# Kernel tuning notes

Hardware: AMD Instinct MI355X
Metric: run time of the kernel (lower is better)

## Reference

```python
import jax, jax.numpy as jnp
import numpy as np

N = 50000
E = 800000
IN, HID, OUT, HEADS = 128, 64, 64, 3
NEG_SLOPE = 0.2
BN_EPS = 1e-5


def setup_inputs() -> dict:
    key = jax.random.key(0)
    ks = jax.random.split(key, 20)
    s = 0.05
    inp = {
        "x": jax.random.normal(ks[0], (N, IN), jnp.float32),
        "edge_index": jax.random.randint(ks[1], (2, E), 0, N, jnp.int32),
        # layer 0: in=128 -> heads=3, C=64 (concat -> 192)
        "Wl0": jax.random.normal(ks[2], (IN, HEADS * HID), jnp.float32) * s,
        "bl0": jnp.zeros((HEADS * HID,), jnp.float32),
        "Wr0": jax.random.normal(ks[3], (IN, HEADS * HID), jnp.float32) * s,
        "br0": jnp.zeros((HEADS * HID,), jnp.float32),
        "att0": jax.random.normal(ks[4], (HEADS, HID), jnp.float32) * s,
        "bias0": jnp.zeros((HEADS * HID,), jnp.float32),
        "gamma0": jnp.ones((HEADS * HID,), jnp.float32),
        "beta0": jnp.zeros((HEADS * HID,), jnp.float32),
        # layer 1: in=192 -> heads=1, C=64
        "Wl1": jax.random.normal(ks[5], (HEADS * HID, OUT), jnp.float32) * s,
        "bl1": jnp.zeros((OUT,), jnp.float32),
        "Wr1": jax.random.normal(ks[6], (HEADS * HID, OUT), jnp.float32) * s,
        "br1": jnp.zeros((OUT,), jnp.float32),
        "att1": jax.random.normal(ks[7], (1, OUT), jnp.float32) * s,
        "bias1": jnp.zeros((OUT,), jnp.float32),
        "gamma1": jnp.ones((OUT,), jnp.float32),
        "beta1": jnp.zeros((OUT,), jnp.float32),
    }
    return inp


def _gatv2_layer(x, Wl, bl, Wr, br, att, bias, src, dst, n):
    H, C = att.shape
    xl = (x @ Wl + bl).reshape(n, H, C)
    xr = (x @ Wr + br).reshape(n, H, C)
    e = jax.nn.leaky_relu(xl[src] + xr[dst], NEG_SLOPE)      # [E,H,C]
    logit = jnp.einsum("ehc,hc->eh", e, att)                 # [E,H]
    m = jax.lax.stop_gradient(jax.ops.segment_max(logit, dst, num_segments=n))
    p = jnp.exp(logit - m[dst])
    denom = jax.ops.segment_sum(p, dst, num_segments=n)
    alpha = p / denom[dst]                                   # per-dst softmax
    out = jax.ops.segment_sum(alpha[:, :, None] * xl[src], dst, num_segments=n)
    return out.reshape(n, H * C) + bias


def _bn(x, gamma, beta):
    mu = x.mean(0)
    var = x.var(0)
    return (x - mu) * jax.lax.rsqrt(var + BN_EPS) * gamma + beta


def reference(x, edge_index, Wl0, bl0, Wr0, br0, att0, bias0, gamma0, beta0,
              Wl1, bl1, Wr1, br1, att1, bias1, gamma1, beta1):
    n = x.shape[0]
    loops = jnp.arange(n, dtype=edge_index.dtype)
    src = jnp.concatenate([edge_index[0], loops])  # PyG add_self_loops=True
    dst = jnp.concatenate([edge_index[1], loops])
    h = _gatv2_layer(x, Wl0, bl0, Wr0, br0, att0, bias0, src, dst, n)
    h = _bn(jax.nn.relu(h), gamma0, beta0)
    h = _gatv2_layer(h, Wl1, bl1, Wr1, br1, att1, bias1, src, dst, n)
    h = _bn(jax.nn.relu(h), gamma1, beta1)
    return h
```

## Files before the change

kernel.cpp:

```cpp
#include <hip/hip_runtime.h>
#include <hip/hip_bf16.h>

#define LRELU_SLOPE 0.2f
#define BN_EPS 1e-5f

typedef __attribute__((ext_vector_type(8))) short short8v;
typedef __attribute__((ext_vector_type(4))) float float4v;

static __device__ __forceinline__ unsigned short f2bf(float f) {
    __hip_bfloat16 b = __float2bfloat16(f);
    return *reinterpret_cast<unsigned short*>(&b);
}
static __device__ __forceinline__ void unpack2(unsigned int u, float& f0, float& f1) {
    f0 = __uint_as_float(u << 16);
    f1 = __uint_as_float(u & 0xffff0000u);
}
static __device__ __forceinline__ float lrelu(float x) {
    return fmaxf(x, LRELU_SLOPE * x);
}

__global__ void convert_w2_kernel(const float* __restrict__ Wl0, const float* __restrict__ Wr0,
                                  const float* __restrict__ Wl1, const float* __restrict__ Wr1,
                                  unsigned short* __restrict__ Wt0, unsigned short* __restrict__ Wt1) {
    int idx = blockIdx.x * blockDim.x + threadIdx.x;
    if (idx < 384 * 128) {
        int c = idx >> 7, k = idx & 127;
        float v = (c < 192) ? Wl0[(size_t)k * 192 + c] : Wr0[(size_t)k * 192 + (c - 192)];
        Wt0[idx] = f2bf(v);
    } else if (idx < 384 * 128 + 128 * 192) {
        int i2 = idx - 384 * 128;
        int c = i2 / 192, k = i2 % 192;
        float v = (c < 64) ? Wl1[(size_t)k * 64 + c] : Wr1[(size_t)k * 64 + (c - 64)];
        Wt1[i2] = f2bf(v);
    }
}

__global__ void count_dst_kernel(const int* __restrict__ dst, int* __restrict__ counts, int E) {
    int e = blockIdx.x * blockDim.x + threadIdx.x;
    if (e < E) atomicAdd(&counts[dst[e]], 1);
}

__global__ void scanA_kernel(const int* __restrict__ counts, int* __restrict__ offs,
                             int* __restrict__ blkSum, int n) {
    __shared__ int wsum[4];
    const int lane = threadIdx.x & 63;
    const int wv = threadIdx.x >> 6;
    int i0 = blockIdx.x * 1024 + (int)threadIdx.x * 4;
    int v0 = (i0 + 0 < n) ? counts[i0 + 0] : 0;
    int v1 = (i0 + 1 < n) ? counts[i0 + 1] : 0;
    int v2 = (i0 + 2 < n) ? counts[i0 + 2] : 0;
    int v3 = (i0 + 3 < n) ? counts[i0 + 3] : 0;
    int s4 = v0 + v1 + v2 + v3;
    int s = s4;
    #pragma unroll
    for (int off = 1; off < 64; off <<= 1) {
        int t = __shfl_up(s, off, 64);
        if (lane >= off) s += t;
    }
    if (lane == 63) wsum[wv] = s;
    __syncthreads();
    int wpre = 0;
    for (int w = 0; w < wv; ++w) wpre += wsum[w];
    int excl = wpre + s - s4;
    if (i0 + 0 < n) offs[i0 + 0] = excl;
    excl += v0;
    if (i0 + 1 < n) offs[i0 + 1] = excl;
    excl += v1;
    if (i0 + 2 < n) offs[i0 + 2] = excl;
    excl += v2;
    if (i0 + 3 < n) offs[i0 + 3] = excl;
    if (threadIdx.x == 255) blkSum[blockIdx.x] = wpre + s;
}

__global__ void scanC_kernel(int* __restrict__ offs, const int* __restrict__ blkSum, int n, int E) {
    __shared__ int baseSh;
    const int b = blockIdx.x;
    if (threadIdx.x < 64) {
        int acc = 0;
        for (int i = threadIdx.x; i < b; i += 64) acc += blkSum[i];
        #pragma unroll
        for (int off = 1; off < 64; off <<= 1) acc += __shfl_xor(acc, off, 64);
        if (threadIdx.x == 0) baseSh = acc;
    }
    __syncthreads();
    const int base = baseSh;
    int i = b * 1024 + (int)threadIdx.x * 4;
    if (i + 3 < n) {
        int4 v = *reinterpret_cast<int4*>(&offs[i]);
        v.x += base; v.y += base; v.z += base; v.w += base;
        *reinterpret_cast<int4*>(&offs[i]) = v;
    } else {
        #pragma unroll
        for (int k = 0; k < 4; ++k)
            if (i + k < n) offs[i + k] += base;
    }
    if (b == 0 && threadIdx.x == 0) offs[n] = E;
}

__global__ void scatter_kernel(const int* __restrict__ src, const int* __restrict__ dst,
                               const int* __restrict__ offs, int* __restrict__ cursor,
                               int* __restrict__ esrc, int E) {
    int e = blockIdx.x * blockDim.x + threadIdx.x;
    if (e < E) {
        int d = dst[e];
        int pos = offs[d] + atomicAdd(&cursor[d], 1);
        esrc[pos] = src[e];
    }
}

template <int K, int NCH, bool BN>
__global__ __launch_bounds__(256) void mfma_dual_gemm(
    const float* __restrict__ X,
    const unsigned short* __restrict__ Wt,
    const float* __restrict__ bl, const float* __restrict__ br,
    const float* __restrict__ stats, const float* __restrict__ gamma,
    const float* __restrict__ beta, float invN,
    unsigned short* __restrict__ xlB, unsigned short* __restrict__ xrB, int N) {
    constexpr int LDA = 40;
    const int rowBase = blockIdx.x * 128;
    const int colBase = blockIdx.y * 128;

    __shared__ unsigned short XS[128 * LDA];
    __shared__ unsigned short WS[128 * LDA];
    __shared__ float ssA[K], ssB[K];

    const int tid = threadIdx.x;
    const int lane = tid & 63;
    const int wv = tid >> 6;
    const int lrow = lane & 15;
    const int lk = lane >> 4;

    if (BN) {
        for (int c = tid; c < K; c += 256) {
            float mu = stats[c] * invN;
            float var = stats[K + c] * invN - mu * mu;
            float sc = gamma[c] * rsqrtf(var + BN_EPS);
            ssA[c] = sc;
            ssB[c] = beta[c] - mu * sc;
        }
        __syncthreads();
    }

    float4v acc[2][8];
    #pragma unroll
    for (int i = 0; i < 2; ++i)
        #pragma unroll
        for (int j = 0; j < 8; ++j) acc[i][j] = (float4v){0.f, 0.f, 0.f, 0.f};

    for (int k0 = 0; k0 < K; k0 += 32) {
        {
            int r = tid >> 3;
            int kq = (tid & 7) * 4;
            float4 sc0, sc1;
            if (BN) {
                sc0 = *reinterpret_cast<const float4*>(&ssA[k0 + kq]);
                sc1 = *reinterpret_cast<const float4*>(&ssB[k0 + kq]);
            }
            #pragma unroll
            for (int i = 0; i < 4; ++i) {
                int row = r + 32 * i;
                int gr = rowBase + row;
                float4 v = make_float4(0.f, 0.f, 0.f, 0.f);
                if (gr < N) v = *reinterpret_cast<const float4*>(&X[(size_t)gr * K + k0 + kq]);
                if (BN) {
                    v.x = v.x * sc0.x + sc1.x;
                    v.y = v.y * sc0.y + sc1.y;
                    v.z = v.z * sc0.z + sc1.z;
                    v.w = v.w * sc0.w + sc1.w;
                }
                ushort4 u;
                u.x = f2bf(v.x); u.y = f2bf(v.y); u.z = f2bf(v.z); u.w = f2bf(v.w);
                *reinterpret_cast<ushort4*>(&XS[row * LDA + kq]) = u;
            }
        }
        {
            int c = tid >> 2;
            int kq8 = (tid & 3) * 8;
            #pragma unroll
            for (int i = 0; i < 2; ++i) {
                int col = c + 64 * i;
                uint4 w = *reinterpret_cast<const uint4*>(&Wt[(size_t)(colBase + col) * K + k0 + kq8]);
                *reinterpret_cast<uint4*>(&WS[col * LDA + kq8]) = w;
            }
        }
        __syncthreads();
        short8v aF[2], bF[8];
        #pragma unroll
        for (int rb = 0; rb < 2; ++rb)
            aF[rb] = *reinterpret_cast<const short8v*>(&XS[(wv * 32 + rb * 16 + lrow) * LDA + lk * 8]);
        #pragma unroll
        for (int cb = 0; cb < 8; ++cb)
            bF[cb] = *reinterpret_cast<const short8v*>(&WS[(cb * 16 + lrow) * LDA + lk * 8]);
        #pragma unroll
        for (int rb = 0; rb < 2; ++rb)
            #pragma unroll
            for (int cb = 0; cb < 8; ++cb)
                acc[rb][cb] = __builtin_amdgcn_mfma_f32_16x16x32_bf16(aF[rb], bF[cb], acc[rb][cb], 0, 0, 0);
        __syncthreads();
    }
    #pragma unroll
    for (int cb = 0; cb < 8; ++cb) {
        int cgG = colBase + cb * 16 + lrow;
        bool isR = cgG >= NCH;
        int cc = isR ? cgG - NCH : cgG;
        int hh = cc >> 6;
        int ch = cc & 63;
        float bv = isR ? br[cc] : bl[cc];
        unsigned short* dstB = (isR ? xrB : xlB) + (size_t)hh * N * 64 + ch;
        #pragma unroll
        for (int rb = 0; rb < 2; ++rb) {
            #pragma unroll
            for (int r = 0; r < 4; ++r) {
                int row = rowBase + wv * 32 + rb * 16 + lk * 4 + r;
                if (row < N) dstB[(size_t)row * 64] = f2bf(acc[rb][cb][r] + bv);
            }
        }
    }
}

template <int H>
__global__ __launch_bounds__(256) void gat_agg_head_kernel(
    const unsigned short* __restrict__ xlB,
    const unsigned short* __restrict__ xrB,
    const int* __restrict__ offs, const int* __restrict__ esrc,
    const float* __restrict__ att,
    const float* __restrict__ bias,
    float* __restrict__ outh,
    int N) {
    const int h = blockIdx.y;
    const unsigned short* xl_ = xlB + (size_t)h * N * 64;
    const unsigned short* xr_ = xrB + (size_t)h * N * 64;
    const int lane = threadIdx.x & 63;
    const int node = blockIdx.x * 4 + (threadIdx.x >> 6);
    if (node >= N) return;
    const int j = lane >> 3;
    const int cg = (lane & 7) * 8;

    float xr[8], at[8], acc[8];
    float den = 0.f;
    {
        uint4 u = *reinterpret_cast<const uint4*>(&xr_[(size_t)node * 64 + cg]);
        unpack2(u.x, xr[0], xr[1]); unpack2(u.y, xr[2], xr[3]);
        unpack2(u.z, xr[4], xr[5]); unpack2(u.w, xr[6], xr[7]);
        float4 a0 = *reinterpret_cast<const float4*>(&att[h * 64 + cg]);
        float4 a1 = *reinterpret_cast<const float4*>(&att[h * 64 + cg + 4]);
        at[0] = a0.x; at[1] = a0.y; at[2] = a0.z; at[3] = a0.w;
        at[4] = a1.x; at[5] = a1.y; at[6] = a1.z; at[7] = a1.w;
        #pragma unroll
        for (int c = 0; c < 8; ++c) acc[c] = 0.f;
    }

    const int beg = offs[node];
    const int total = offs[node + 1] - beg + 1;
    uint4 u0, u1;
    {
        int vc = (j < total) ? j : (total - 1);
        int s0 = (vc == 0) ? node : esrc[beg + vc - 1];
        u0 = *reinterpret_cast<const uint4*>(&xl_[(size_t)s0 * 64 + cg]);
        int v1i = j + 8;
        int vc1 = (v1i < total) ? v1i : (total - 1);
        int s1 = (vc1 == 0) ? node : esrc[beg + vc1 - 1];
        u1 = *reinterpret_cast<const uint4*>(&xl_[(size_t)s1 * 64 + cg]);
    }
    for (int t = 0; t < total; t += 8) {
        float xlv[8];
        unpack2(u0.x, xlv[0], xlv[1]); unpack2(u0.y, xlv[2], xlv[3]);
        unpack2(u0.z, xlv[4], xlv[5]); unpack2(u0.w, xlv[6], xlv[7]);
        u0 = u1;
        const int v2 = t + 16 + j;
        if (v2 < total) {
            int s2 = esrc[beg + v2 - 1];
            u1 = *reinterpret_cast<const uint4*>(&xl_[(size_t)s2 * 64 + cg]);
        }
        float s = 0.f;
        #pragma unroll
        for (int c = 0; c < 8; ++c) s += lrelu(xlv[c] + xr[c]) * at[c];
        #pragma unroll
        for (int off = 1; off <= 4; off <<= 1) s += __shfl_xor(s, off, 64);
        const float w = (t + j < total) ? 1.f : 0.f;
        float p = w * __expf(s);
        den += p;
        #pragma unroll
        for (int c = 0; c < 8; ++c) acc[c] += p * xlv[c];
    }

    #pragma unroll
    for (int off = 8; off <= 32; off <<= 1) {
        den += __shfl_xor(den, off, 64);
        #pragma unroll
        for (int c = 0; c < 8; ++c) acc[c] += __shfl_xor(acc[c], off, 64);
    }

    if (j == 0) {
        float inv = 1.f / den;
        float4 b0 = *reinterpret_cast<const float4*>(&bias[h * 64 + cg]);
        float4 b1 = *reinterpret_cast<const float4*>(&bias[h * 64 + cg + 4]);
        float4 o0, o1;
        o0.x = fmaxf(acc[0] * inv + b0.x, 0.f); o0.y = fmaxf(acc[1] * inv + b0.y, 0.f);
        o0.z = fmaxf(acc[2] * inv + b0.z, 0.f); o0.w = fmaxf(acc[3] * inv + b0.w, 0.f);
        o1.x = fmaxf(acc[4] * inv + b1.x, 0.f); o1.y = fmaxf(acc[5] * inv + b1.y, 0.f);
        o1.z = fmaxf(acc[6] * inv + b1.z, 0.f); o1.w = fmaxf(acc[7] * inv + b1.w, 0.f);
        float* orow = &outh[(size_t)node * (H * 64) + h * 64 + cg];
        *reinterpret_cast<float4*>(orow) = o0;
        *reinterpret_cast<float4*>(orow + 4) = o1;
    }
}

template <int CH>
__global__ void bn_stats_kernel(const float* __restrict__ h, float* __restrict__ stats, int N) {
    const int c = threadIdx.x;
    float s = 0.f, q = 0.f;
    for (int r = blockIdx.x; r < N; r += gridDim.x) {
        float v = h[(size_t)r * CH + c];
        s += v;
        q += v * v;
    }
    atomicAdd(&stats[c], s);
    atomicAdd(&stats[CH + c], q);
}

__global__ void bn_finapply64_kernel(float* __restrict__ h, const float* __restrict__ stats,
                                     const float* __restrict__ gamma, const float* __restrict__ beta,
                                     float invN, size_t total4) {
    size_t i = (size_t)blockIdx.x * blockDim.x + threadIdx.x;
    if (i >= total4) return;
    size_t e = i * 4;
    int c = (int)(e & 63);
    float4 v = *reinterpret_cast<float4*>(&h[e]);
    #pragma unroll
    for (int k = 0; k < 4; ++k) {
        float mu = stats[c + k] * invN;
        float var = stats[64 + c + k] * invN - mu * mu;
        float sc = gamma[c + k] * rsqrtf(var + BN_EPS);
        (&v.x)[k] = ((&v.x)[k] - mu) * sc + beta[c + k];
    }
    *reinterpret_cast<float4*>(&h[e]) = v;
}

extern "C" void kernel_launch(void* const* d_in, const int* in_sizes, int n_in,
                              void* d_out, int out_size, void* d_ws, size_t ws_size,
                              hipStream_t stream) {
    const float* x     = (const float*)d_in[0];
    const int*   eidx  = (const int*)d_in[1];
    const float* Wl0   = (const float*)d_in[2];
    const float* bl0   = (const float*)d_in[3];
    const float* Wr0   = (const float*)d_in[4];
    const float* br0   = (const float*)d_in[5];
    const float* att0  = (const float*)d_in[6];
    const float* bias0 = (const float*)d_in[7];
    const float* g0    = (const float*)d_in[8];
    const float* be0   = (const float*)d_in[9];
    const float* Wl1   = (const float*)d_in[10];
    const float* bl1   = (const float*)d_in[11];
    const float* Wr1   = (const float*)d_in[12];
    const float* br1   = (const float*)d_in[13];
    const float* att1  = (const float*)d_in[14];
    const float* bias1 = (const float*)d_in[15];
    const float* g1    = (const float*)d_in[16];
    const float* be1   = (const float*)d_in[17];

    const int N = in_sizes[0] / 128;
    const int E = in_sizes[1] / 2;
    const int* srcIdx = eidx;
    const int* dstIdx = eidx + E;
    const int nChunks = (N + 1023) >> 10;
    const int nGroups = (N + 3) / 4;
    const float invN = 1.f / (float)N;

    char* base = (char*)d_ws;
    auto alloc = [&](size_t bytes) {
        char* p = base;
        base += (bytes + 255) & ~(size_t)255;
        return p;
    };
    unsigned short* projL = (unsigned short*)alloc((size_t)3 * N * 64 * 2);
    unsigned short* projR = (unsigned short*)alloc((size_t)3 * N * 64 * 2);
    float* h0    = (float*)alloc((size_t)N * 192 * 4);
    int*   offs  = (int*)alloc((size_t)(N + 1) * 4);
    int*   esrc  = (int*)alloc((size_t)E * 4);
    int*   blkSum= (int*)alloc((size_t)nChunks * 4);
    unsigned short* Wt0 = (unsigned short*)alloc((size_t)384 * 128 * 2);
    unsigned short* Wt1 = (unsigned short*)alloc((size_t)128 * 192 * 2);
    char* zeroBeg = base;
    int*   counts = (int*)alloc((size_t)N * 4);
    int*   cursor = (int*)alloc((size_t)N * 4);
    float* stats0 = (float*)alloc(384 * 4);
    float* stats1 = (float*)alloc(128 * 4);
    size_t zeroBytes = (size_t)(base - zeroBeg);

    hipMemsetAsync(zeroBeg, 0, zeroBytes, stream);
    convert_w2_kernel<<<(384 * 128 + 128 * 192 + 255) / 256, 256, 0, stream>>>(Wl0, Wr0, Wl1, Wr1, Wt0, Wt1);

    count_dst_kernel<<<(E + 255) / 256, 256, 0, stream>>>(dstIdx, counts, E);
    scanA_kernel<<<nChunks, 256, 0, stream>>>(counts, offs, blkSum, N);
    scanC_kernel<<<nChunks, 256, 0, stream>>>(offs, blkSum, N, E);
    scatter_kernel<<<(E + 255) / 256, 256, 0, stream>>>(srcIdx, dstIdx, offs, cursor, esrc, E);

    {
        dim3 grid((N + 127) / 128, 3);
        mfma_dual_gemm<128, 192, false><<<grid, 256, 0, stream>>>(
            x, Wt0, bl0, br0, nullptr, nullptr, nullptr, 0.f, projL, projR, N);
    }
    {
        dim3 grid(nGroups, 3);
        gat_agg_head_kernel<3><<<grid, 256, 0, stream>>>(projL, projR, offs, esrc, att0, bias0, h0, N);
    }
    bn_stats_kernel<192><<<256, 192, 0, stream>>>(h0, stats0, N);

    {
        dim3 grid((N + 127) / 128, 1);
        mfma_dual_gemm<192, 64, true><<<grid, 256, 0, stream>>>(
            h0, Wt1, bl1, br1, stats0, g0, be0, invN, projL, projR, N);
    }
    float* out = (float*)d_out;
    {
        dim3 grid(nGroups, 1);
        gat_agg_head_kernel<1><<<grid, 256, 0, stream>>>(projL, projR, offs, esrc, att1, bias1, out, N);
    }
    bn_stats_kernel<64><<<256, 64, 0, stream>>>(out, stats1, N);
    {
        size_t tot4 = (size_t)N * 16;
        bn_finapply64_kernel<<<(unsigned)((tot4 + 255) / 256), 256, 0, stream>>>(out, stats1, g1, be1, invN, tot4);
    }
}
```

Baseline: 382.1 us.

## Stage GEMM epilogue through LDS for vectorized stores; fuse weight conversion with degree count

The GEMM epilogue now writes bf16 results into a per-wave LDS tile that reuses the XS/WS shared buffer, then reads 16-byte chunks and stores them to global memory as coalesced uint4 writes instead of scattered 2-byte stores. Separately, the weight-conversion kernel and the destination-count kernel are merged into one launch to save a kernel launch. This costs extra LDS traffic and a reuse of the staging buffer, which relies on the final __syncthreads of the main loop.

```diff
diff --git a/kernel.cpp b/kernel.cpp
--- a/kernel.cpp
+++ b/kernel.cpp
@@ -19,9 +19,10 @@
     return fmaxf(x, LRELU_SLOPE * x);
 }
 
-__global__ void convert_w2_kernel(const float* __restrict__ Wl0, const float* __restrict__ Wr0,
-                                  const float* __restrict__ Wl1, const float* __restrict__ Wr1,
-                                  unsigned short* __restrict__ Wt0, unsigned short* __restrict__ Wt1) {
+__global__ void convcount_kernel(const float* __restrict__ Wl0, const float* __restrict__ Wr0,
+                                 const float* __restrict__ Wl1, const float* __restrict__ Wr1,
+                                 unsigned short* __restrict__ Wt0, unsigned short* __restrict__ Wt1,
+                                 const int* __restrict__ dst, int* __restrict__ counts, int E) {
     int idx = blockIdx.x * blockDim.x + threadIdx.x;
     if (idx < 384 * 128) {
         int c = idx >> 7, k = idx & 127;
@@ -33,11 +34,7 @@
         float v = (c < 64) ? Wl1[(size_t)k * 64 + c] : Wr1[(size_t)k * 64 + (c - 64)];
         Wt1[i2] = f2bf(v);
     }
-}
-
-__global__ void count_dst_kernel(const int* __restrict__ dst, int* __restrict__ counts, int E) {
-    int e = blockIdx.x * blockDim.x + threadIdx.x;
-    if (e < E) atomicAdd(&counts[dst[e]], 1);
+    if (idx < E) atomicAdd(&counts[dst[idx]], 1);
 }
 
 __global__ void scanA_kernel(const int* __restrict__ counts, int* __restrict__ offs,
@@ -120,8 +117,9 @@
     const int rowBase = blockIdx.x * 128;
     const int colBase = blockIdx.y * 128;
 
-    __shared__ unsigned short XS[128 * LDA];
-    __shared__ unsigned short WS[128 * LDA];
+    __shared__ unsigned short SH[16896];
+    unsigned short* XS = SH;
+    unsigned short* WS = SH + 128 * LDA;
     __shared__ float ssA[K], ssB[K];
 
     const int tid = threadIdx.x;
@@ -198,22 +196,38 @@
                 acc[rb][cb] = __builtin_amdgcn_mfma_f32_16x16x32_bf16(aF[rb], bF[cb], acc[rb][cb], 0, 0, 0);
         __syncthreads();
     }
+
+    unsigned short* TR = SH + wv * (32 * 132);
     #pragma unroll
     for (int cb = 0; cb < 8; ++cb) {
         int cgG = colBase + cb * 16 + lrow;
         bool isR = cgG >= NCH;
         int cc = isR ? cgG - NCH : cgG;
-        int hh = cc >> 6;
-        int ch = cc & 63;
         float bv = isR ? br[cc] : bl[cc];
-        unsigned short* dstB = (isR ? xrB : xlB) + (size_t)hh * N * 64 + ch;
         #pragma unroll
         for (int rb = 0; rb < 2; ++rb) {
             #pragma unroll
             for (int r = 0; r < 4; ++r) {
-                int row = rowBase + wv * 32 + rb * 16 + lk * 4 + r;
-                if (row < N) dstB[(size_t)row * 64] = f2bf(acc[rb][cb][r] + bv);
+                int lr = rb * 16 + lk * 4 + r;
+                TR[lr * 132 + cb * 16 + lrow] = f2bf(acc[rb][cb][r] + bv);
             }
+        }
+    }
+    #pragma unroll
+    for (int it = 0; it < 8; ++it) {
+        int idx = it * 64 + lane;
+        int lr = idx >> 4;
+        int ck = (idx & 15) * 8;
+        int grow = rowBase + wv * 32 + lr;
+        if (grow < N) {
+            uint4 v = *reinterpret_cast<const uint4*>(&TR[lr * 132 + ck]);
+            int cgG = colBase + ck;
+            bool isR = cgG >= NCH;
+            int cc = isR ? cgG - NCH : cgG;
+            int hh = cc >> 6;
+            int ch = cc & 63;
+            unsigned short* dstB = (isR ? xrB : xlB) + (size_t)hh * N * 64 + (size_t)grow * 64 + ch;
+            *reinterpret_cast<uint4*>(dstB) = v;
         }
     }
 }
@@ -389,9 +403,11 @@
     size_t zeroBytes = (size_t)(base - zeroBeg);
 
     hipMemsetAsync(zeroBeg, 0, zeroBytes, stream);
-    convert_w2_kernel<<<(384 * 128 + 128 * 192 + 255) / 256, 256, 0, stream>>>(Wl0, Wr0, Wl1, Wr1, Wt0, Wt1);
-
-    count_dst_kernel<<<(E + 255) / 256, 256, 0, stream>>>(dstIdx, counts, E);
+
+    {
+        int work = E > (384 * 128 + 128 * 192) ? E : (384 * 128 + 128 * 192);
+        convcount_kernel<<<(work + 255) / 256, 256, 0, stream>>>(Wl0, Wr0, Wl1, Wr1, Wt0, Wt1, dstIdx, counts, E);
+    }
     scanA_kernel<<<nChunks, 256, 0, stream>>>(counts, offs, blkSum, N);
     scanC_kernel<<<nChunks, 256, 0, stream>>>(offs, blkSum, N, E);
     scatter_kernel<<<(E + 255) / 256, 256, 0, stream>>>(srcIdx, dstIdx, offs, cursor, esrc, E);
```

After: 363.9 us. 1.05x faster.
